# Kernel optimization log

Hardware: AMD Instinct MI355X
Metric: run time of the kernel (lower is better)

The kernel has to match this reference:

```python
import jax, jax.numpy as jnp
import numpy as np

N_NODES = 50000


def setup_inputs() -> dict:
    key = jax.random.key(0)
    ks = jax.random.split(key, 6)
    L, d = 3, 128
    x = jax.random.normal(ks[0], (N_NODES, d), dtype=jnp.float32)
    edge_index = jax.random.randint(ks[1], (2, 640000), 0, N_NODES, dtype=jnp.int64)
    s = 1.0 / np.sqrt(d)
    W1 = jax.random.normal(ks[2], (L, d, d), dtype=jnp.float32) * s
    W2 = jax.random.normal(ks[3], (L, d, d), dtype=jnp.float32) * s
    b1 = jnp.zeros((L, d), dtype=jnp.float32)
    b2 = jnp.zeros((L, d), dtype=jnp.float32)
    eps = jnp.zeros((L,), dtype=jnp.float32)
    final_w = jax.random.normal(ks[4], (d + L * d, d), dtype=jnp.float32) / np.sqrt(d + L * d)
    final_b = jnp.zeros((d,), dtype=jnp.float32)
    return {"x": x, "edge_index": edge_index, "W1": W1, "b1": b1,
            "W2": W2, "b2": b2, "eps": eps, "final_w": final_w, "final_b": final_b}


def reference(x, edge_index, W1, b1, W2, b2, eps, final_w, final_b):
    src, dst = edge_index[0], edge_index[1]
    num_layers = W1.shape[0]
    xs = [x]
    h = x
    for l in range(num_layers):
        # GINConv: sum-aggregate neighbor features, add (1+eps)*self, then 2-layer MLP
        agg = jax.ops.segment_sum(h[src], dst, num_segments=N_NODES)  # [N, d]
        z = (1.0 + eps[l]) * h + agg
        z = jax.nn.relu(z @ W1[l] + b1[l])
        h = jax.nn.relu(z @ W2[l] + b2[l])
        xs.append(h)
    out = jnp.concatenate(xs, axis=-1)  # [N, in + L*out]
    return out @ final_w + final_b
```

## Files before the change

### kernel.cpp

```cpp
#include <hip/hip_runtime.h>

#define NNODES 50000
#define NEDGES 640000
#define D 128

typedef unsigned short u16;
typedef unsigned int u32;
typedef __bf16 bf16x8 __attribute__((ext_vector_type(8)));
typedef float f32x4 __attribute__((ext_vector_type(4)));
union AB { uint4 u4; bf16x8 f; };

__device__ __forceinline__ u16 f2b(float f) {
    u32 u = __float_as_uint(f);
    return (u16)((u + 0x7fffu + ((u >> 16) & 1u)) >> 16);
}
__device__ __forceinline__ u32 pack2(float lo, float hi) {
    return (u32)f2b(lo) | ((u32)f2b(hi) << 16);
}
__device__ __forceinline__ float blo(u32 v) { return __uint_as_float(v << 16); }
__device__ __forceinline__ float bhi(u32 v) { return __uint_as_float(v & 0xffff0000u); }

__device__ __forceinline__ void acc8(float* a, uint4 v) {
    a[0] += blo(v.x); a[1] += bhi(v.x);
    a[2] += blo(v.y); a[3] += bhi(v.y);
    a[4] += blo(v.z); a[5] += bhi(v.z);
    a[6] += blo(v.w); a[7] += bhi(v.w);
}


__global__ void k_hist(const int* __restrict__ dst, int* __restrict__ cnt) {
    int e = blockIdx.x * 256 + threadIdx.x;
    if (e < NEDGES) atomicAdd(&cnt[dst[e]], 1);
}

__global__ void k_scan1(const int* __restrict__ cnt, int* __restrict__ rp,
                        int* __restrict__ bsum) {
    __shared__ int s[256];
    int tid = threadIdx.x;
    int i = blockIdx.x * 256 + tid;
    int v = (i < NNODES) ? cnt[i] : 0;
    s[tid] = v;
    __syncthreads();
    for (int off = 1; off < 256; off <<= 1) {
        int t = (tid >= off) ? s[tid - off] : 0;
        __syncthreads();
        s[tid] += t;
        __syncthreads();
    }
    if (i < NNODES) rp[i] = s[tid] - v;
    if (tid == 255) bsum[blockIdx.x] = s[255];
}

__global__ void k_scan2(int* __restrict__ bsum, int nb) {
    __shared__ int s[256];
    int tid = threadIdx.x;
    int v = (tid < nb) ? bsum[tid] : 0;
    s[tid] = v;
    __syncthreads();
    for (int off = 1; off < 256; off <<= 1) {
        int t = (tid >= off) ? s[tid - off] : 0;
        __syncthreads();
        s[tid] += t;
        __syncthreads();
    }
    if (tid < nb) bsum[tid] = s[tid] - v;
}

__global__ void k_add(int* __restrict__ rp, const int* __restrict__ bsum) {
    int i = blockIdx.x * 256 + threadIdx.x;
    if (i < NNODES) rp[i] += bsum[blockIdx.x];
    if (i == 0) rp[NNODES] = NEDGES;
}

__global__ void k_scatter(const int* __restrict__ src, const int* __restrict__ dst,
                          const int* __restrict__ rp, int* __restrict__ cnt,
                          int* __restrict__ srcs) {
    int e = blockIdx.x * 256 + threadIdx.x;
    if (e < NEDGES) {
        int dn = dst[e];
        int old = atomicSub(&cnt[dn], 1);
        srcs[rp[dn] + old - 1] = src[e];
    }
}

__global__ void k_prep(const float* __restrict__ W1, const float* __restrict__ W2,
                       const float* __restrict__ fw, const float* __restrict__ x,
                       u16* __restrict__ wT1, u16* __restrict__ wT2,
                       u16* __restrict__ fwTc, u32* __restrict__ xb) {
    int idx = blockIdx.x * 256 + threadIdx.x;
    if (idx < 3 * 16384) {
        int l = idx >> 14, r = idx & 16383, n = r >> 7, k = r & 127;
        wT1[idx] = f2b(W1[l * 16384 + k * 128 + n]);
        wT2[idx] = f2b(W2[l * 16384 + k * 128 + n]);
    }
    if (idx < 4 * 16384) {
        int ch = idx >> 14, r = idx & 16383, n = r >> 7, k = r & 127;
        fwTc[idx] = f2b(fw[(ch * 128 + k) * 128 + n]);
    }
    if (idx < NNODES * 64) {
        float2 v = ((const float2*)x)[idx];
        xb[idx] = pack2(v.x, v.y);
    }
}

__global__ void k_agg(const uint4* __restrict__ h4, const int* __restrict__ rp,
                      const int* __restrict__ srcs, const float* __restrict__ epsp,
                      uint4* __restrict__ z4) {
    int tid = threadIdx.x;
    int c = tid & 15;
    int node = (blockIdx.x * 256 + tid) >> 4;
    int gbase = tid & 48;
    float sc = 1.0f + epsp[0];

    uint4 sv = h4[node * 16 + c];
    float acc[8];
    acc[0] = sc * blo(sv.x); acc[1] = sc * bhi(sv.x);
    acc[2] = sc * blo(sv.y); acc[3] = sc * bhi(sv.y);
    acc[4] = sc * blo(sv.z); acc[5] = sc * bhi(sv.z);
    acc[6] = sc * blo(sv.w); acc[7] = sc * bhi(sv.w);

    int beg = rp[node], end = rp[node + 1];
    for (int base = beg; base < end; base += 16) {
        int n = end - base; if (n > 16) n = 16;
        int myidx = (base + c < end) ? srcs[base + c] : 0;
        int j = 0;
        for (; j + 8 <= n; j += 8) {
            int s0 = __shfl(myidx, gbase + j + 0, 64);
            int s1 = __shfl(myidx, gbase + j + 1, 64);
            int s2 = __shfl(myidx, gbase + j + 2, 64);
            int s3 = __shfl(myidx, gbase + j + 3, 64);
            int s4 = __shfl(myidx, gbase + j + 4, 64);
            int s5 = __shfl(myidx, gbase + j + 5, 64);
            int s6 = __shfl(myidx, gbase + j + 6, 64);
            int s7 = __shfl(myidx, gbase + j + 7, 64);
            uint4 v0 = h4[s0 * 16 + c]; uint4 v1 = h4[s1 * 16 + c];
            uint4 v2 = h4[s2 * 16 + c]; uint4 v3 = h4[s3 * 16 + c];
            uint4 v4 = h4[s4 * 16 + c]; uint4 v5 = h4[s5 * 16 + c];
            uint4 v6 = h4[s6 * 16 + c]; uint4 v7 = h4[s7 * 16 + c];
            acc8(acc, v0); acc8(acc, v1); acc8(acc, v2); acc8(acc, v3);
            acc8(acc, v4); acc8(acc, v5); acc8(acc, v6); acc8(acc, v7);
        }
        for (; j + 4 <= n; j += 4) {
            int s0 = __shfl(myidx, gbase + j + 0, 64);
            int s1 = __shfl(myidx, gbase + j + 1, 64);
            int s2 = __shfl(myidx, gbase + j + 2, 64);
            int s3 = __shfl(myidx, gbase + j + 3, 64);
            uint4 v0 = h4[s0 * 16 + c]; uint4 v1 = h4[s1 * 16 + c];
            uint4 v2 = h4[s2 * 16 + c]; uint4 v3 = h4[s3 * 16 + c];
            acc8(acc, v0); acc8(acc, v1); acc8(acc, v2); acc8(acc, v3);
        }
        for (; j < n; ++j) {
            int s0 = __shfl(myidx, gbase + j, 64);
            uint4 v0 = h4[s0 * 16 + c];
            acc8(acc, v0);
        }
    }

    uint4 o;
    o.x = pack2(acc[0], acc[1]); o.y = pack2(acc[2], acc[3]);
    o.z = pack2(acc[4], acc[5]); o.w = pack2(acc[6], acc[7]);
    z4[node * 16 + c] = o;
}

__launch_bounds__(256, 2)
__global__ void k_mlp(const u16* __restrict__ A, const u16* __restrict__ wT1g,
                      const float* __restrict__ b1, const u16* __restrict__ wT2g,
                      const float* __restrict__ b2, u16* __restrict__ H) {
    __shared__ u16 Tb[128 * 128];
    __shared__ u16 wbuf[128 * 128];
    uint4* Tb4 = (uint4*)Tb;
    uint4* wb4 = (uint4*)wbuf;
    int tid = threadIdx.x;
    int r0 = blockIdx.x * 128;
    int wave = tid >> 6, lane = tid & 63, l16 = lane & 15, quad = lane >> 4;

    {
        const uint4* g = (const uint4*)wT1g;
        for (int i = tid; i < 2048; i += 256) {
            int n = i >> 4, ch = i & 15;
            wb4[n * 16 + ((ch + n) & 15)] = g[i];
        }
    }

    AB a[2][4];
#pragma unroll
    for (int s = 0; s < 2; ++s) {
        int row = r0 + wave * 32 + s * 16 + l16;
#pragma unroll
        for (int kb = 0; kb < 4; ++kb) {
            if (row < NNODES)
                a[s][kb].u4 = *(const uint4*)&A[row * 128 + kb * 32 + quad * 8];
            else
                a[s][kb].u4 = make_uint4(0, 0, 0, 0);
        }
    }
    __syncthreads();

    f32x4 acc[2][8];
#pragma unroll
    for (int col = 0; col < 8; ++col) {
        float bv = b1[col * 16 + l16];
        acc[0][col] = (f32x4){bv, bv, bv, bv};
        acc[1][col] = (f32x4){bv, bv, bv, bv};
    }
#pragma unroll
    for (int col = 0; col < 8; ++col) {
#pragma unroll
        for (int kb = 0; kb < 4; ++kb) {
            AB b;
            int n = col * 16 + l16;
            b.u4 = wb4[n * 16 + ((kb * 4 + quad + n) & 15)];
            acc[0][col] = __builtin_amdgcn_mfma_f32_16x16x32_bf16(a[0][kb].f, b.f, acc[0][col], 0, 0, 0);
            acc[1][col] = __builtin_amdgcn_mfma_f32_16x16x32_bf16(a[1][kb].f, b.f, acc[1][col], 0, 0, 0);
        }
    }

#pragma unroll
    for (int s = 0; s < 2; ++s)
#pragma unroll
        for (int col = 0; col < 8; ++col)
#pragma unroll
            for (int r = 0; r < 4; ++r) {
                int row = wave * 32 + s * 16 + quad * 4 + r;
                int kcol = col * 16 + l16;
                int ch = kcol >> 3;
                Tb[row * 128 + ((ch + row) & 15) * 8 + (kcol & 7)] =
                    f2b(fmaxf(acc[s][col][r], 0.f));
            }
    __syncthreads();

    {
        const uint4* g = (const uint4*)wT2g;
        for (int i = tid; i < 2048; i += 256) {
            int n = i >> 4, ch = i & 15;
            wb4[n * 16 + ((ch + n) & 15)] = g[i];
        }
    }
    AB a2[2][4];
#pragma unroll
    for (int s = 0; s < 2; ++s) {
        int m = wave * 32 + s * 16 + l16;
#pragma unroll
        for (int kb = 0; kb < 4; ++kb)
            a2[s][kb].u4 = Tb4[m * 16 + ((kb * 4 + quad + m) & 15)];
    }
    __syncthreads();

#pragma unroll
    for (int col = 0; col < 8; ++col) {
        float bv = b2[col * 16 + l16];
        acc[0][col] = (f32x4){bv, bv, bv, bv};
        acc[1][col] = (f32x4){bv, bv, bv, bv};
    }
#pragma unroll
    for (int col = 0; col < 8; ++col) {
#pragma unroll
        for (int kb = 0; kb < 4; ++kb) {
            AB b;
            int n = col * 16 + l16;
            b.u4 = wb4[n * 16 + ((kb * 4 + quad + n) & 15)];
            acc[0][col] = __builtin_amdgcn_mfma_f32_16x16x32_bf16(a2[0][kb].f, b.f, acc[0][col], 0, 0, 0);
            acc[1][col] = __builtin_amdgcn_mfma_f32_16x16x32_bf16(a2[1][kb].f, b.f, acc[1][col], 0, 0, 0);
        }
    }
    __syncthreads();

#pragma unroll
    for (int s = 0; s < 2; ++s)
#pragma unroll
        for (int col = 0; col < 8; ++col)
#pragma unroll
            for (int r = 0; r < 4; ++r) {
                int row = wave * 32 + s * 16 + quad * 4 + r;
                int kcol = col * 16 + l16;
                int ch = kcol >> 3;
                Tb[row * 128 + ((ch + row) & 15) * 8 + (kcol & 7)] =
                    f2b(fmaxf(acc[s][col][r], 0.f));
            }
    __syncthreads();

    for (int i = tid; i < 2048; i += 256) {
        int r = i >> 4, ch = i & 15;
        int grow = r0 + r;
        if (grow < NNODES)
            *(uint4*)&H[grow * 128 + ch * 8] = Tb4[r * 16 + ((ch + r) & 15)];
    }
}

__launch_bounds__(256, 2)
__global__ void k_final(const u16* __restrict__ xb, const u16* __restrict__ h1,
                        const u16* __restrict__ h2b, const u16* __restrict__ h3,
                        const u16* __restrict__ fwTc, const float* __restrict__ fb,
                        float* __restrict__ out) {
    __shared__ u16 wbuf[128 * 128];
    uint4* wb4 = (uint4*)wbuf;
    int tid = threadIdx.x;
    int wave = tid >> 6, lane = tid & 63, l16 = lane & 15, quad = lane >> 4;
    int r0 = blockIdx.x * 128 + wave * 32;

    f32x4 acc[2][8];
#pragma unroll
    for (int col = 0; col < 8; ++col) {
        float bv = fb[col * 16 + l16];
        acc[0][col] = (f32x4){bv, bv, bv, bv};
        acc[1][col] = (f32x4){bv, bv, bv, bv};
    }

    const u16* chin[4] = {xb, h1, h2b, h3};
    for (int chn = 0; chn < 4; ++chn) {
        __syncthreads();
        {
            const uint4* g = (const uint4*)(fwTc + chn * 16384);
            for (int i = tid; i < 2048; i += 256) {
                int n = i >> 4, ch = i & 15;
                wb4[n * 16 + ((ch + n) & 15)] = g[i];
            }
        }
        const u16* cp = chin[chn];
        AB a[2][4];
#pragma unroll
        for (int s = 0; s < 2; ++s) {
            int row = r0 + s * 16 + l16;
#pragma unroll
            for (int kb = 0; kb < 4; ++kb) {
                if (row < NNODES)
                    a[s][kb].u4 = *(const uint4*)&cp[row * 128 + kb * 32 + quad * 8];
                else
                    a[s][kb].u4 = make_uint4(0, 0, 0, 0);
            }
        }
        __syncthreads();
#pragma unroll
        for (int col = 0; col < 8; ++col) {
#pragma unroll
            for (int kb = 0; kb < 4; ++kb) {
                AB b;
                int n = col * 16 + l16;
                b.u4 = wb4[n * 16 + ((kb * 4 + quad + n) & 15)];
                acc[0][col] = __builtin_amdgcn_mfma_f32_16x16x32_bf16(a[0][kb].f, b.f, acc[0][col], 0, 0, 0);
                acc[1][col] = __builtin_amdgcn_mfma_f32_16x16x32_bf16(a[1][kb].f, b.f, acc[1][col], 0, 0, 0);
            }
        }
    }

#pragma unroll
    for (int s = 0; s < 2; ++s)
#pragma unroll
        for (int col = 0; col < 8; ++col)
#pragma unroll
            for (int r = 0; r < 4; ++r) {
                int row = r0 + s * 16 + quad * 4 + r;
                if (row < NNODES) out[row * 128 + col * 16 + l16] = acc[s][col][r];
            }
}

extern "C" void kernel_launch(void* const* d_in, const int* in_sizes, int n_in,
                              void* d_out, int out_size, void* d_ws, size_t ws_size,
                              hipStream_t stream) {
    const float* x   = (const float*)d_in[0];
    const int*   ei  = (const int*)d_in[1];
    const float* W1  = (const float*)d_in[2];
    const float* b1  = (const float*)d_in[3];
    const float* W2  = (const float*)d_in[4];
    const float* b2  = (const float*)d_in[5];
    const float* eps = (const float*)d_in[6];
    const float* fw  = (const float*)d_in[7];
    const float* fb  = (const float*)d_in[8];
    float* out = (float*)d_out;

    const int* srcA = ei;
    const int* dstA = ei + NEDGES;

    char* p = (char*)d_ws;
    size_t off = 0;
    auto take = [&](size_t bytes) {
        char* r = p + off;
        off = (off + bytes + 255) & ~(size_t)255;
        return r;
    };
    int* rp   = (int*)take((NNODES + 1) * sizeof(int));
    int* cnt  = (int*)take(NNODES * sizeof(int));
    int* bsum = (int*)take(256 * sizeof(int));
    int* srcs = (int*)take(NEDGES * sizeof(int));
    u16* wT1  = (u16*)take(3 * 16384 * sizeof(u16));
    u16* wT2  = (u16*)take(3 * 16384 * sizeof(u16));
    u16* fwTc = (u16*)take(4 * 16384 * sizeof(u16));
    u16* xb   = (u16*)take((size_t)NNODES * D * sizeof(u16));
    u16* zb   = (u16*)take((size_t)NNODES * D * sizeof(u16));
    u16* hb1  = (u16*)take((size_t)NNODES * D * sizeof(u16));
    u16* hb2  = (u16*)take((size_t)NNODES * D * sizeof(u16));
    u16* hb3  = (u16*)take((size_t)NNODES * D * sizeof(u16));
    (void)ws_size; (void)in_sizes; (void)n_in; (void)out_size;

    hipMemsetAsync(cnt, 0, NNODES * sizeof(int), stream);

    int nb = (NNODES + 255) / 256;
    k_hist<<<(NEDGES + 255) / 256, 256, 0, stream>>>(dstA, cnt);
    k_scan1<<<nb, 256, 0, stream>>>(cnt, rp, bsum);
    k_scan2<<<1, 256, 0, stream>>>(bsum, nb);
    k_add<<<nb, 256, 0, stream>>>(rp, bsum);
    k_scatter<<<(NEDGES + 255) / 256, 256, 0, stream>>>(srcA, dstA, rp, cnt, srcs);
    k_prep<<<(NNODES * 64 + 255) / 256, 256, 0, stream>>>(W1, W2, fw, x, wT1, wT2, fwTc, (u32*)xb);

    const u16* hin = xb;
    u16* houts[3] = {hb1, hb2, hb3};
    int gm = (NNODES + 127) / 128;
    for (int l = 0; l < 3; ++l) {
        k_agg<<<NNODES * 16 / 256, 256, 0, stream>>>((const uint4*)hin, rp, srcs, eps + l, (uint4*)zb);
        k_mlp<<<gm, 256, 0, stream>>>(zb, wT1 + l * 16384, b1 + l * D,
                                      wT2 + l * 16384, b2 + l * D, houts[l]);
        hin = houts[l];
    }
    k_final<<<gm, 256, 0, stream>>>(xb, hb1, hb2, hb3, fwTc, fb, out);
}
```

Baseline: 298.7 us.

## Shrink MLP and final GEMM tiles to 16 rows per wave, read weights from global

The MLP and final projection kernels now give each wave its own 16-row tile instead of 32 rows per wave in a 128-row block. Weight B fragments are loaded straight from global memory (relying on L1/L2 hits) rather than staged into 32KB of shared memory behind block barriers, and the per-wave intermediate uses a small padded shared scratch. The aim is to remove the __syncthreads, cut LDS use and register pressure so more waves fit, and to spread work over more blocks. The cost is more global weight traffic per row processed and half the weight reuse per fragment load.

```diff
diff --git a/kernel.cpp b/kernel.cpp
--- a/kernel.cpp
+++ b/kernel.cpp
@@ -162,196 +162,127 @@
     z4[node * 16 + c] = o;
 }
 
-__launch_bounds__(256, 2)
+#define SROW 136
+__launch_bounds__(256)
 __global__ void k_mlp(const u16* __restrict__ A, const u16* __restrict__ wT1g,
                       const float* __restrict__ b1, const u16* __restrict__ wT2g,
                       const float* __restrict__ b2, u16* __restrict__ H) {
-    __shared__ u16 Tb[128 * 128];
-    __shared__ u16 wbuf[128 * 128];
-    uint4* Tb4 = (uint4*)Tb;
-    uint4* wb4 = (uint4*)wbuf;
-    int tid = threadIdx.x;
-    int r0 = blockIdx.x * 128;
+    __shared__ u16 scratch[4][16 * SROW];
+    int tid = threadIdx.x;
     int wave = tid >> 6, lane = tid & 63, l16 = lane & 15, quad = lane >> 4;
-
-    {
-        const uint4* g = (const uint4*)wT1g;
-        for (int i = tid; i < 2048; i += 256) {
-            int n = i >> 4, ch = i & 15;
-            wb4[n * 16 + ((ch + n) & 15)] = g[i];
-        }
-    }
-
-    AB a[2][4];
-#pragma unroll
-    for (int s = 0; s < 2; ++s) {
-        int row = r0 + wave * 32 + s * 16 + l16;
-#pragma unroll
-        for (int kb = 0; kb < 4; ++kb) {
-            if (row < NNODES)
-                a[s][kb].u4 = *(const uint4*)&A[row * 128 + kb * 32 + quad * 8];
-            else
-                a[s][kb].u4 = make_uint4(0, 0, 0, 0);
-        }
-    }
-    __syncthreads();
-
-    f32x4 acc[2][8];
+    int wid = blockIdx.x * 4 + wave;
+    if (wid * 16 >= NNODES) return;
+    int r0 = wid * 16;
+    u16* sc = scratch[wave];
+
+    AB a[4];
+#pragma unroll
+    for (int kb = 0; kb < 4; ++kb)
+        a[kb].u4 = *(const uint4*)&A[(r0 + l16) * 128 + kb * 32 + quad * 8];
+
+    f32x4 acc[8];
 #pragma unroll
     for (int col = 0; col < 8; ++col) {
         float bv = b1[col * 16 + l16];
-        acc[0][col] = (f32x4){bv, bv, bv, bv};
-        acc[1][col] = (f32x4){bv, bv, bv, bv};
-    }
-#pragma unroll
-    for (int col = 0; col < 8; ++col) {
-#pragma unroll
-        for (int kb = 0; kb < 4; ++kb) {
-            AB b;
-            int n = col * 16 + l16;
-            b.u4 = wb4[n * 16 + ((kb * 4 + quad + n) & 15)];
-            acc[0][col] = __builtin_amdgcn_mfma_f32_16x16x32_bf16(a[0][kb].f, b.f, acc[0][col], 0, 0, 0);
-            acc[1][col] = __builtin_amdgcn_mfma_f32_16x16x32_bf16(a[1][kb].f, b.f, acc[1][col], 0, 0, 0);
-        }
-    }
-
-#pragma unroll
-    for (int s = 0; s < 2; ++s)
-#pragma unroll
-        for (int col = 0; col < 8; ++col)
-#pragma unroll
-            for (int r = 0; r < 4; ++r) {
-                int row = wave * 32 + s * 16 + quad * 4 + r;
-                int kcol = col * 16 + l16;
-                int ch = kcol >> 3;
-                Tb[row * 128 + ((ch + row) & 15) * 8 + (kcol & 7)] =
-                    f2b(fmaxf(acc[s][col][r], 0.f));
-            }
-    __syncthreads();
-
-    {
-        const uint4* g = (const uint4*)wT2g;
-        for (int i = tid; i < 2048; i += 256) {
-            int n = i >> 4, ch = i & 15;
-            wb4[n * 16 + ((ch + n) & 15)] = g[i];
-        }
-    }
-    AB a2[2][4];
-#pragma unroll
-    for (int s = 0; s < 2; ++s) {
-        int m = wave * 32 + s * 16 + l16;
-#pragma unroll
-        for (int kb = 0; kb < 4; ++kb)
-            a2[s][kb].u4 = Tb4[m * 16 + ((kb * 4 + quad + m) & 15)];
-    }
-    __syncthreads();
+        acc[col] = (f32x4){bv, bv, bv, bv};
+    }
+#pragma unroll
+    for (int col = 0; col < 8; ++col) {
+        AB b[4];
+#pragma unroll
+        for (int kb = 0; kb < 4; ++kb)
+            b[kb].u4 = *(const uint4*)&wT1g[(col * 16 + l16) * 128 + kb * 32 + quad * 8];
+#pragma unroll
+        for (int kb = 0; kb < 4; ++kb)
+            acc[col] = __builtin_amdgcn_mfma_f32_16x16x32_bf16(a[kb].f, b[kb].f, acc[col], 0, 0, 0);
+    }
+
+#pragma unroll
+    for (int col = 0; col < 8; ++col)
+#pragma unroll
+        for (int r = 0; r < 4; ++r)
+            sc[(quad * 4 + r) * SROW + col * 16 + l16] = f2b(fmaxf(acc[col][r], 0.f));
+
+    AB a2[4];
+#pragma unroll
+    for (int kb = 0; kb < 4; ++kb)
+        a2[kb].u4 = *(const uint4*)&sc[l16 * SROW + kb * 32 + quad * 8];
 
 #pragma unroll
     for (int col = 0; col < 8; ++col) {
         float bv = b2[col * 16 + l16];
-        acc[0][col] = (f32x4){bv, bv, bv, bv};
-        acc[1][col] = (f32x4){bv, bv, bv, bv};
-    }
-#pragma unroll
-    for (int col = 0; col < 8; ++col) {
-#pragma unroll
-        for (int kb = 0; kb < 4; ++kb) {
-            AB b;
-            int n = col * 16 + l16;
-            b.u4 = wb4[n * 16 + ((kb * 4 + quad + n) & 15)];
-            acc[0][col] = __builtin_amdgcn_mfma_f32_16x16x32_bf16(a2[0][kb].f, b.f, acc[0][col], 0, 0, 0);
-            acc[1][col] = __builtin_amdgcn_mfma_f32_16x16x32_bf16(a2[1][kb].f, b.f, acc[1][col], 0, 0, 0);
-        }
-    }
-    __syncthreads();
-
-#pragma unroll
-    for (int s = 0; s < 2; ++s)
-#pragma unroll
-        for (int col = 0; col < 8; ++col)
-#pragma unroll
-            for (int r = 0; r < 4; ++r) {
-                int row = wave * 32 + s * 16 + quad * 4 + r;
-                int kcol = col * 16 + l16;
-                int ch = kcol >> 3;
-                Tb[row * 128 + ((ch + row) & 15) * 8 + (kcol & 7)] =
-                    f2b(fmaxf(acc[s][col][r], 0.f));
-            }
-    __syncthreads();
-
-    for (int i = tid; i < 2048; i += 256) {
-        int r = i >> 4, ch = i & 15;
-        int grow = r0 + r;
-        if (grow < NNODES)
-            *(uint4*)&H[grow * 128 + ch * 8] = Tb4[r * 16 + ((ch + r) & 15)];
-    }
-}
-
-__launch_bounds__(256, 2)
+        acc[col] = (f32x4){bv, bv, bv, bv};
+    }
+#pragma unroll
+    for (int col = 0; col < 8; ++col) {
+        AB b[4];
+#pragma unroll
+        for (int kb = 0; kb < 4; ++kb)
+            b[kb].u4 = *(const uint4*)&wT2g[(col * 16 + l16) * 128 + kb * 32 + quad * 8];
+#pragma unroll
+        for (int kb = 0; kb < 4; ++kb)
+            acc[col] = __builtin_amdgcn_mfma_f32_16x16x32_bf16(a2[kb].f, b[kb].f, acc[col], 0, 0, 0);
+    }
+
+#pragma unroll
+    for (int col = 0; col < 8; ++col)
+#pragma unroll
+        for (int r = 0; r < 4; ++r)
+            sc[(quad * 4 + r) * SROW + col * 16 + l16] = f2b(fmaxf(acc[col][r], 0.f));
+
+#pragma unroll
+    for (int p = 0; p < 4; ++p) {
+        int idx = p * 64 + lane;
+        int row = idx >> 4, ch = idx & 15;
+        uint4 v = *(const uint4*)&sc[row * SROW + ch * 8];
+        *(uint4*)&H[(r0 + row) * 128 + ch * 8] = v;
+    }
+}
+
+__launch_bounds__(256)
 __global__ void k_final(const u16* __restrict__ xb, const u16* __restrict__ h1,
                         const u16* __restrict__ h2b, const u16* __restrict__ h3,
                         const u16* __restrict__ fwTc, const float* __restrict__ fb,
                         float* __restrict__ out) {
-    __shared__ u16 wbuf[128 * 128];
-    uint4* wb4 = (uint4*)wbuf;
     int tid = threadIdx.x;
     int wave = tid >> 6, lane = tid & 63, l16 = lane & 15, quad = lane >> 4;
-    int r0 = blockIdx.x * 128 + wave * 32;
-
-    f32x4 acc[2][8];
+    int wid = blockIdx.x * 4 + wave;
+    if (wid * 16 >= NNODES) return;
+    int r0 = wid * 16;
+
+    f32x4 acc[8];
 #pragma unroll
     for (int col = 0; col < 8; ++col) {
         float bv = fb[col * 16 + l16];
-        acc[0][col] = (f32x4){bv, bv, bv, bv};
-        acc[1][col] = (f32x4){bv, bv, bv, bv};
+        acc[col] = (f32x4){bv, bv, bv, bv};
     }
 
     const u16* chin[4] = {xb, h1, h2b, h3};
+#pragma unroll
     for (int chn = 0; chn < 4; ++chn) {
-        __syncthreads();
-        {
-            const uint4* g = (const uint4*)(fwTc + chn * 16384);
-            for (int i = tid; i < 2048; i += 256) {
-                int n = i >> 4, ch = i & 15;
-                wb4[n * 16 + ((ch + n) & 15)] = g[i];
-            }
+        const u16* cp = chin[chn];
+        const u16* wp = fwTc + chn * 16384;
+        AB a[4];
+#pragma unroll
+        for (int kb = 0; kb < 4; ++kb)
+            a[kb].u4 = *(const uint4*)&cp[(r0 + l16) * 128 + kb * 32 + quad * 8];
+#pragma unroll
+        for (int col = 0; col < 8; ++col) {
+            AB b[4];
+#pragma unroll
+            for (int kb = 0; kb < 4; ++kb)
+                b[kb].u4 = *(const uint4*)&wp[(col * 16 + l16) * 128 + kb * 32 + quad * 8];
+#pragma unroll
+            for (int kb = 0; kb < 4; ++kb)
+                acc[col] = __builtin_amdgcn_mfma_f32_16x16x32_bf16(a[kb].f, b[kb].f, acc[col], 0, 0, 0);
         }
-        const u16* cp = chin[chn];
-        AB a[2][4];
-#pragma unroll
-        for (int s = 0; s < 2; ++s) {
-            int row = r0 + s * 16 + l16;
-#pragma unroll
-            for (int kb = 0; kb < 4; ++kb) {
-                if (row < NNODES)
-                    a[s][kb].u4 = *(const uint4*)&cp[row * 128 + kb * 32 + quad * 8];
-                else
-                    a[s][kb].u4 = make_uint4(0, 0, 0, 0);
-            }
-        }
-        __syncthreads();
-#pragma unroll
-        for (int col = 0; col < 8; ++col) {
-#pragma unroll
-            for (int kb = 0; kb < 4; ++kb) {
-                AB b;
-                int n = col * 16 + l16;
-                b.u4 = wb4[n * 16 + ((kb * 4 + quad + n) & 15)];
-                acc[0][col] = __builtin_amdgcn_mfma_f32_16x16x32_bf16(a[0][kb].f, b.f, acc[0][col], 0, 0, 0);
-                acc[1][col] = __builtin_amdgcn_mfma_f32_16x16x32_bf16(a[1][kb].f, b.f, acc[1][col], 0, 0, 0);
-            }
-        }
-    }
-
-#pragma unroll
-    for (int s = 0; s < 2; ++s)
-#pragma unroll
-        for (int col = 0; col < 8; ++col)
-#pragma unroll
-            for (int r = 0; r < 4; ++r) {
-                int row = r0 + s * 16 + quad * 4 + r;
-                if (row < NNODES) out[row * 128 + col * 16 + l16] = acc[s][col][r];
-            }
+    }
+
+#pragma unroll
+    for (int col = 0; col < 8; ++col)
+#pragma unroll
+        for (int r = 0; r < 4; ++r)
+            out[(r0 + quad * 4 + r) * 128 + col * 16 + l16] = acc[col][r];
 }
 
 extern "C" void kernel_launch(void* const* d_in, const int* in_sizes, int n_in,
@@ -404,12 +335,12 @@
 
     const u16* hin = xb;
     u16* houts[3] = {hb1, hb2, hb3};
-    int gm = (NNODES + 127) / 128;
+    int gw = (3125 + 3) / 4;
     for (int l = 0; l < 3; ++l) {
         k_agg<<<NNODES * 16 / 256, 256, 0, stream>>>((const uint4*)hin, rp, srcs, eps + l, (uint4*)zb);
-        k_mlp<<<gm, 256, 0, stream>>>(zb, wT1 + l * 16384, b1 + l * D,
+        k_mlp<<<gw, 256, 0, stream>>>(zb, wT1 + l * 16384, b1 + l * D,
                                       wT2 + l * 16384, b2 + l * D, houts[l]);
         hin = houts[l];
     }
-    k_final<<<gm, 256, 0, stream>>>(xb, hb1, hb2, hb3, fwTc, fb, out);
-}
+    k_final<<<gw, 256, 0, stream>>>(xb, hb1, hb2, hb3, fwTc, fb, out);
+}
```

Measured after the change: 405.5 us. +35.8%, slower.

## Shrink MLP/final tiles to 64 rows and stream pre-swizzled weights via LDS DMA

Applied to the files above, without the earlier changes.

Weights are pre-laid out in k_prep in an MFMA-fragment order split into two 64-column halves, so each half can be copied straight into LDS with global_load_lds. The MLP and final kernels now handle 64 rows per block, with each wave owning a 16-column slice across all rows instead of 32 rows across all columns. LDS use is halved and launch bounds rise to 3 blocks per SM. The intent is to cut the weight-staging cost, raise occupancy and double the grid size. In exchange, each block loads the weights twice as often and adds extra barriers.

```diff
diff --git a/kernel.cpp b/kernel.cpp
--- a/kernel.cpp
+++ b/kernel.cpp
@@ -9,6 +9,13 @@
 typedef __bf16 bf16x8 __attribute__((ext_vector_type(8)));
 typedef float f32x4 __attribute__((ext_vector_type(4)));
 union AB { uint4 u4; bf16x8 f; };
+
+#define AS1 __attribute__((address_space(1)))
+#define AS3 __attribute__((address_space(3)))
+
+__device__ __forceinline__ void dma16(const u16* g, u16* l) {
+    __builtin_amdgcn_global_load_lds((const AS1 u32*)g, (AS3 u32*)l, 16, 0, 0);
+}
 
 __device__ __forceinline__ u16 f2b(float f) {
     u32 u = __float_as_uint(f);
@@ -85,17 +92,26 @@
 
 __global__ void k_prep(const float* __restrict__ W1, const float* __restrict__ W2,
                        const float* __restrict__ fw, const float* __restrict__ x,
-                       u16* __restrict__ wT1, u16* __restrict__ wT2,
-                       u16* __restrict__ fwTc, u32* __restrict__ xb) {
+                       u16* __restrict__ w1x, u16* __restrict__ w2x,
+                       u16* __restrict__ fwx, u32* __restrict__ xb) {
     int idx = blockIdx.x * 256 + threadIdx.x;
     if (idx < 3 * 16384) {
-        int l = idx >> 14, r = idx & 16383, n = r >> 7, k = r & 127;
-        wT1[idx] = f2b(W1[l * 16384 + k * 128 + n]);
-        wT2[idx] = f2b(W2[l * 16384 + k * 128 + n]);
+        int l = idx >> 14, r = idx & 16383;
+        int h = r >> 13, r2 = r & 8191;
+        int t = r2 >> 9, r3 = r2 & 511;
+        int c = r3 >> 3, e = r3 & 7;
+        int k = (t >> 2) * 32 + (t & 3) * 8 + e;
+        int n = h * 64 + c;
+        w1x[idx] = f2b(W1[l * 16384 + k * 128 + n]);
+        w2x[idx] = f2b(W2[l * 16384 + k * 128 + n]);
     }
     if (idx < 4 * 16384) {
-        int ch = idx >> 14, r = idx & 16383, n = r >> 7, k = r & 127;
-        fwTc[idx] = f2b(fw[(ch * 128 + k) * 128 + n]);
+        int chn = idx >> 14, r = idx & 16383;
+        int h = r >> 13, r2 = r & 8191;
+        int t = r2 >> 9, r3 = r2 & 511;
+        int c = r3 >> 3, e = r3 & 7;
+        int k = (t >> 2) * 32 + (t & 3) * 8 + e;
+        fwx[idx] = f2b(fw[(chn * 128 + k) * 128 + h * 64 + c]);
     }
     if (idx < NNODES * 64) {
         float2 v = ((const float2*)x)[idx];
@@ -162,124 +178,138 @@
     z4[node * 16 + c] = o;
 }
 
-__launch_bounds__(256, 2)
-__global__ void k_mlp(const u16* __restrict__ A, const u16* __restrict__ wT1g,
-                      const float* __restrict__ b1, const u16* __restrict__ wT2g,
+__launch_bounds__(256, 3)
+__global__ void k_mlp(const u16* __restrict__ A, const u16* __restrict__ w1x,
+                      const float* __restrict__ b1, const u16* __restrict__ w2x,
                       const float* __restrict__ b2, u16* __restrict__ H) {
-    __shared__ u16 Tb[128 * 128];
-    __shared__ u16 wbuf[128 * 128];
+    __shared__ __align__(16) u16 Tb[64 * 128];
+    __shared__ __align__(16) u16 wb[8192];
     uint4* Tb4 = (uint4*)Tb;
-    uint4* wb4 = (uint4*)wbuf;
     int tid = threadIdx.x;
-    int r0 = blockIdx.x * 128;
     int wave = tid >> 6, lane = tid & 63, l16 = lane & 15, quad = lane >> 4;
-
-    {
-        const uint4* g = (const uint4*)wT1g;
-        for (int i = tid; i < 2048; i += 256) {
-            int n = i >> 4, ch = i & 15;
-            wb4[n * 16 + ((ch + n) & 15)] = g[i];
-        }
-    }
-
-    AB a[2][4];
-#pragma unroll
-    for (int s = 0; s < 2; ++s) {
-        int row = r0 + wave * 32 + s * 16 + l16;
-#pragma unroll
-        for (int kb = 0; kb < 4; ++kb) {
-            if (row < NNODES)
-                a[s][kb].u4 = *(const uint4*)&A[row * 128 + kb * 32 + quad * 8];
-            else
-                a[s][kb].u4 = make_uint4(0, 0, 0, 0);
-        }
-    }
-    __syncthreads();
-
-    f32x4 acc[2][8];
-#pragma unroll
-    for (int col = 0; col < 8; ++col) {
-        float bv = b1[col * 16 + l16];
-        acc[0][col] = (f32x4){bv, bv, bv, bv};
-        acc[1][col] = (f32x4){bv, bv, bv, bv};
-    }
-#pragma unroll
-    for (int col = 0; col < 8; ++col) {
-#pragma unroll
-        for (int kb = 0; kb < 4; ++kb) {
-            AB b;
-            int n = col * 16 + l16;
-            b.u4 = wb4[n * 16 + ((kb * 4 + quad + n) & 15)];
-            acc[0][col] = __builtin_amdgcn_mfma_f32_16x16x32_bf16(a[0][kb].f, b.f, acc[0][col], 0, 0, 0);
-            acc[1][col] = __builtin_amdgcn_mfma_f32_16x16x32_bf16(a[1][kb].f, b.f, acc[1][col], 0, 0, 0);
-        }
-    }
-
-#pragma unroll
-    for (int s = 0; s < 2; ++s)
-#pragma unroll
-        for (int col = 0; col < 8; ++col)
+    int r0 = blockIdx.x * 64;
+
+    AB a[4][4];
+#pragma unroll
+    for (int s = 0; s < 4; ++s) {
+        int row = r0 + s * 16 + l16;
+#pragma unroll
+        for (int kb = 0; kb < 4; ++kb)
+            a[s][kb].u4 = (row < NNODES)
+                ? *(const uint4*)&A[row * 128 + kb * 32 + quad * 8]
+                : make_uint4(0, 0, 0, 0);
+    }
+#pragma unroll
+    for (int p = 0; p < 4; ++p) {
+        int seg = p * 4 + wave;
+        dma16(w1x + seg * 512 + lane * 8, wb + seg * 512);
+    }
+    __syncthreads();
+
+    f32x4 acc[2][4];
+#pragma unroll
+    for (int h = 0; h < 2; ++h) {
+        float bv = b1[(h * 4 + wave) * 16 + l16];
+#pragma unroll
+        for (int s = 0; s < 4; ++s) acc[h][s] = (f32x4){bv, bv, bv, bv};
+    }
+#pragma unroll
+    for (int kb = 0; kb < 4; ++kb) {
+        AB b; b.u4 = *(const uint4*)&wb[(kb * 4 + quad) * 512 + (wave * 16 + l16) * 8];
+#pragma unroll
+        for (int s = 0; s < 4; ++s)
+            acc[0][s] = __builtin_amdgcn_mfma_f32_16x16x32_bf16(a[s][kb].f, b.f, acc[0][s], 0, 0, 0);
+    }
+    __syncthreads();
+#pragma unroll
+    for (int p = 0; p < 4; ++p) {
+        int seg = p * 4 + wave;
+        dma16(w1x + 8192 + seg * 512 + lane * 8, wb + seg * 512);
+    }
+    __syncthreads();
+#pragma unroll
+    for (int kb = 0; kb < 4; ++kb) {
+        AB b; b.u4 = *(const uint4*)&wb[(kb * 4 + quad) * 512 + (wave * 16 + l16) * 8];
+#pragma unroll
+        for (int s = 0; s < 4; ++s)
+            acc[1][s] = __builtin_amdgcn_mfma_f32_16x16x32_bf16(a[s][kb].f, b.f, acc[1][s], 0, 0, 0);
+    }
+
+#pragma unroll
+    for (int h = 0; h < 2; ++h) {
+        int kcol = (h * 4 + wave) * 16 + l16;
+        int ch = kcol >> 3;
+#pragma unroll
+        for (int s = 0; s < 4; ++s)
 #pragma unroll
             for (int r = 0; r < 4; ++r) {
-                int row = wave * 32 + s * 16 + quad * 4 + r;
-                int kcol = col * 16 + l16;
-                int ch = kcol >> 3;
+                int row = s * 16 + quad * 4 + r;
                 Tb[row * 128 + ((ch + row) & 15) * 8 + (kcol & 7)] =
-                    f2b(fmaxf(acc[s][col][r], 0.f));
+                    f2b(fmaxf(acc[h][s][r], 0.f));
             }
-    __syncthreads();
-
-    {
-        const uint4* g = (const uint4*)wT2g;
-        for (int i = tid; i < 2048; i += 256) {
-            int n = i >> 4, ch = i & 15;
-            wb4[n * 16 + ((ch + n) & 15)] = g[i];
-        }
-    }
-    AB a2[2][4];
-#pragma unroll
-    for (int s = 0; s < 2; ++s) {
-        int m = wave * 32 + s * 16 + l16;
+    }
+    __syncthreads();
+
+#pragma unroll
+    for (int p = 0; p < 4; ++p) {
+        int seg = p * 4 + wave;
+        dma16(w2x + seg * 512 + lane * 8, wb + seg * 512);
+    }
+#pragma unroll
+    for (int s = 0; s < 4; ++s) {
+        int m = s * 16 + l16;
 #pragma unroll
         for (int kb = 0; kb < 4; ++kb)
-            a2[s][kb].u4 = Tb4[m * 16 + ((kb * 4 + quad + m) & 15)];
-    }
-    __syncthreads();
-
-#pragma unroll
-    for (int col = 0; col < 8; ++col) {
-        float bv = b2[col * 16 + l16];
-        acc[0][col] = (f32x4){bv, bv, bv, bv};
-        acc[1][col] = (f32x4){bv, bv, bv, bv};
-    }
-#pragma unroll
-    for (int col = 0; col < 8; ++col) {
-#pragma unroll
-        for (int kb = 0; kb < 4; ++kb) {
-            AB b;
-            int n = col * 16 + l16;
-            b.u4 = wb4[n * 16 + ((kb * 4 + quad + n) & 15)];
-            acc[0][col] = __builtin_amdgcn_mfma_f32_16x16x32_bf16(a2[0][kb].f, b.f, acc[0][col], 0, 0, 0);
-            acc[1][col] = __builtin_amdgcn_mfma_f32_16x16x32_bf16(a2[1][kb].f, b.f, acc[1][col], 0, 0, 0);
-        }
-    }
-    __syncthreads();
-
-#pragma unroll
-    for (int s = 0; s < 2; ++s)
-#pragma unroll
-        for (int col = 0; col < 8; ++col)
+            a[s][kb].u4 = Tb4[m * 16 + ((kb * 4 + quad + m) & 15)];
+    }
+    __syncthreads();
+
+#pragma unroll
+    for (int h = 0; h < 2; ++h) {
+        float bv = b2[(h * 4 + wave) * 16 + l16];
+#pragma unroll
+        for (int s = 0; s < 4; ++s) acc[h][s] = (f32x4){bv, bv, bv, bv};
+    }
+#pragma unroll
+    for (int kb = 0; kb < 4; ++kb) {
+        AB b; b.u4 = *(const uint4*)&wb[(kb * 4 + quad) * 512 + (wave * 16 + l16) * 8];
+#pragma unroll
+        for (int s = 0; s < 4; ++s)
+            acc[0][s] = __builtin_amdgcn_mfma_f32_16x16x32_bf16(a[s][kb].f, b.f, acc[0][s], 0, 0, 0);
+    }
+    __syncthreads();
+#pragma unroll
+    for (int p = 0; p < 4; ++p) {
+        int seg = p * 4 + wave;
+        dma16(w2x + 8192 + seg * 512 + lane * 8, wb + seg * 512);
+    }
+    __syncthreads();
+#pragma unroll
+    for (int kb = 0; kb < 4; ++kb) {
+        AB b; b.u4 = *(const uint4*)&wb[(kb * 4 + quad) * 512 + (wave * 16 + l16) * 8];
+#pragma unroll
+        for (int s = 0; s < 4; ++s)
+            acc[1][s] = __builtin_amdgcn_mfma_f32_16x16x32_bf16(a[s][kb].f, b.f, acc[1][s], 0, 0, 0);
+    }
+
+#pragma unroll
+    for (int h = 0; h < 2; ++h) {
+        int kcol = (h * 4 + wave) * 16 + l16;
+        int ch = kcol >> 3;
+#pragma unroll
+        for (int s = 0; s < 4; ++s)
 #pragma unroll
             for (int r = 0; r < 4; ++r) {
-                int row = wave * 32 + s * 16 + quad * 4 + r;
-                int kcol = col * 16 + l16;
-                int ch = kcol >> 3;
+                int row = s * 16 + quad * 4 + r;
                 Tb[row * 128 + ((ch + row) & 15) * 8 + (kcol & 7)] =
-                    f2b(fmaxf(acc[s][col][r], 0.f));
+                    f2b(fmaxf(acc[h][s][r], 0.f));
             }
-    __syncthreads();
-
-    for (int i = tid; i < 2048; i += 256) {
+    }
+    __syncthreads();
+
+#pragma unroll
+    for (int p = 0; p < 4; ++p) {
+        int i = p * 256 + tid;
         int r = i >> 4, ch = i & 15;
         int grow = r0 + r;
         if (grow < NNODES)
@@ -287,70 +317,66 @@
     }
 }
 
-__launch_bounds__(256, 2)
+__launch_bounds__(256, 3)
 __global__ void k_final(const u16* __restrict__ xb, const u16* __restrict__ h1,
                         const u16* __restrict__ h2b, const u16* __restrict__ h3,
-                        const u16* __restrict__ fwTc, const float* __restrict__ fb,
+                        const u16* __restrict__ fwx, const float* __restrict__ fb,
                         float* __restrict__ out) {
-    __shared__ u16 wbuf[128 * 128];
-    uint4* wb4 = (uint4*)wbuf;
+    __shared__ __align__(16) u16 wb[8192];
     int tid = threadIdx.x;
     int wave = tid >> 6, lane = tid & 63, l16 = lane & 15, quad = lane >> 4;
-    int r0 = blockIdx.x * 128 + wave * 32;
-
-    f32x4 acc[2][8];
-#pragma unroll
-    for (int col = 0; col < 8; ++col) {
-        float bv = fb[col * 16 + l16];
-        acc[0][col] = (f32x4){bv, bv, bv, bv};
-        acc[1][col] = (f32x4){bv, bv, bv, bv};
+    int r0 = blockIdx.x * 64;
+
+    f32x4 acc[2][4];
+#pragma unroll
+    for (int h = 0; h < 2; ++h) {
+        float bv = fb[(h * 4 + wave) * 16 + l16];
+#pragma unroll
+        for (int s = 0; s < 4; ++s) acc[h][s] = (f32x4){bv, bv, bv, bv};
     }
 
     const u16* chin[4] = {xb, h1, h2b, h3};
+#pragma unroll
     for (int chn = 0; chn < 4; ++chn) {
-        __syncthreads();
-        {
-            const uint4* g = (const uint4*)(fwTc + chn * 16384);
-            for (int i = tid; i < 2048; i += 256) {
-                int n = i >> 4, ch = i & 15;
-                wb4[n * 16 + ((ch + n) & 15)] = g[i];
+        const u16* cp = chin[chn];
+        AB a[4][4];
+#pragma unroll
+        for (int s = 0; s < 4; ++s) {
+            int row = r0 + s * 16 + l16;
+#pragma unroll
+            for (int kb = 0; kb < 4; ++kb)
+                a[s][kb].u4 = (row < NNODES)
+                    ? *(const uint4*)&cp[row * 128 + kb * 32 + quad * 8]
+                    : make_uint4(0, 0, 0, 0);
+        }
+#pragma unroll
+        for (int h = 0; h < 2; ++h) {
+            __syncthreads();
+#pragma unroll
+            for (int p = 0; p < 4; ++p) {
+                int seg = p * 4 + wave;
+                dma16(fwx + (chn * 2 + h) * 8192 + seg * 512 + lane * 8, wb + seg * 512);
+            }
+            __syncthreads();
+#pragma unroll
+            for (int kb = 0; kb < 4; ++kb) {
+                AB b; b.u4 = *(const uint4*)&wb[(kb * 4 + quad) * 512 + (wave * 16 + l16) * 8];
+#pragma unroll
+                for (int s = 0; s < 4; ++s)
+                    acc[h][s] = __builtin_amdgcn_mfma_f32_16x16x32_bf16(a[s][kb].f, b.f, acc[h][s], 0, 0, 0);
             }
         }
-        const u16* cp = chin[chn];
-        AB a[2][4];
-#pragma unroll
-        for (int s = 0; s < 2; ++s) {
-            int row = r0 + s * 16 + l16;
-#pragma unroll
-            for (int kb = 0; kb < 4; ++kb) {
-                if (row < NNODES)
-                    a[s][kb].u4 = *(const uint4*)&cp[row * 128 + kb * 32 + quad * 8];
-                else
-                    a[s][kb].u4 = make_uint4(0, 0, 0, 0);
-            }
-        }
-        __syncthreads();
-#pragma unroll
-        for (int col = 0; col < 8; ++col) {
-#pragma unroll
-            for (int kb = 0; kb < 4; ++kb) {
-                AB b;
-                int n = col * 16 + l16;
-                b.u4 = wb4[n * 16 + ((kb * 4 + quad + n) & 15)];
-                acc[0][col] = __builtin_amdgcn_mfma_f32_16x16x32_bf16(a[0][kb].f, b.f, acc[0][col], 0, 0, 0);
-                acc[1][col] = __builtin_amdgcn_mfma_f32_16x16x32_bf16(a[1][kb].f, b.f, acc[1][col], 0, 0, 0);
-            }
-        }
-    }
-
-#pragma unroll
-    for (int s = 0; s < 2; ++s)
-#pragma unroll
-        for (int col = 0; col < 8; ++col)
+    }
+
+#pragma unroll
+    for (int h = 0; h < 2; ++h)
+#pragma unroll
+        for (int s = 0; s < 4; ++s)
 #pragma unroll
             for (int r = 0; r < 4; ++r) {
                 int row = r0 + s * 16 + quad * 4 + r;
-                if (row < NNODES) out[row * 128 + col * 16 + l16] = acc[s][col][r];
+                if (row < NNODES)
+                    out[row * 128 + (h * 4 + wave) * 16 + l16] = acc[h][s][r];
             }
 }
 
@@ -382,9 +408,9 @@
     int* cnt  = (int*)take(NNODES * sizeof(int));
     int* bsum = (int*)take(256 * sizeof(int));
     int* srcs = (int*)take(NEDGES * sizeof(int));
-    u16* wT1  = (u16*)take(3 * 16384 * sizeof(u16));
-    u16* wT2  = (u16*)take(3 * 16384 * sizeof(u16));
-    u16* fwTc = (u16*)take(4 * 16384 * sizeof(u16));
+    u16* w1x  = (u16*)take(3 * 16384 * sizeof(u16));
+    u16* w2x  = (u16*)take(3 * 16384 * sizeof(u16));
+    u16* fwx  = (u16*)take(4 * 16384 * sizeof(u16));
     u16* xb   = (u16*)take((size_t)NNODES * D * sizeof(u16));
     u16* zb   = (u16*)take((size_t)NNODES * D * sizeof(u16));
     u16* hb1  = (u16*)take((size_t)NNODES * D * sizeof(u16));
@@ -400,16 +426,16 @@
     k_scan2<<<1, 256, 0, stream>>>(bsum, nb);
     k_add<<<nb, 256, 0, stream>>>(rp, bsum);
     k_scatter<<<(NEDGES + 255) / 256, 256, 0, stream>>>(srcA, dstA, rp, cnt, srcs);
-    k_prep<<<(NNODES * 64 + 255) / 256, 256, 0, stream>>>(W1, W2, fw, x, wT1, wT2, fwTc, (u32*)xb);
+    k_prep<<<(NNODES * 64 + 255) / 256, 256, 0, stream>>>(W1, W2, fw, x, w1x, w2x, fwx, (u32*)xb);
 
     const u16* hin = xb;
     u16* houts[3] = {hb1, hb2, hb3};
-    int gm = (NNODES + 127) / 128;
+    int gm = (NNODES + 63) / 64;
     for (int l = 0; l < 3; ++l) {
         k_agg<<<NNODES * 16 / 256, 256, 0, stream>>>((const uint4*)hin, rp, srcs, eps + l, (uint4*)zb);
-        k_mlp<<<gm, 256, 0, stream>>>(zb, wT1 + l * 16384, b1 + l * D,
-                                      wT2 + l * 16384, b2 + l * D, houts[l]);
+        k_mlp<<<gm, 256, 0, stream>>>(zb, w1x + l * 16384, b1 + l * D,
+                                      w2x + l * 16384, b2 + l * D, houts[l]);
         hin = houts[l];
     }
-    k_final<<<gm, 256, 0, stream>>>(xb, hb1, hb2, hb3, fwTc, fb, out);
-}
+    k_final<<<gm, 256, 0, stream>>>(xb, hb1, hb2, hb3, fwx, fb, out);
+}
```

Result: slower. 327.1 us (+9.5%).
